# Kernel tuning notes

Hardware: AMD Instinct MI355X
Metric: run time of the kernel (lower is better)

## Reference

```python
import jax, jax.numpy as jnp
import numpy as np
from jax import lax

NMS_RADIUS = 3
DN = ('NCHW', 'OIHW', 'NCHW')


def _conv(x, w, b):
    # 3x3 or 1x1 conv, stride 1, SAME padding (matches padding=k//2 in torch)
    return lax.conv_general_dilated(x, w, (1, 1), 'SAME', dimension_numbers=DN) + b[None, :, None, None]


def _pool2(x):
    # 2x2 max pool, stride 2
    return lax.reduce_window(x, -jnp.inf, lax.max, (1, 1, 2, 2), (1, 1, 2, 2), 'VALID')


def simple_nms(scores, nms_radius):
    # scores: [b, H, W]. Iterative max-pool based NMS (2 suppression rounds).
    k = 2 * nms_radius + 1

    def mp(x):
        return lax.reduce_window(x, -jnp.inf, lax.max, (1, k, k), (1, 1, 1), 'SAME')

    zeros = jnp.zeros_like(scores)
    max_mask = scores == mp(scores)
    for _ in range(2):
        supp_mask = mp(max_mask.astype(scores.dtype)) > 0
        supp_scores = jnp.where(supp_mask, zeros, scores)
        new_max_mask = supp_scores == mp(supp_scores)
        max_mask = max_mask | (new_max_mask & ~supp_mask)
    return jnp.where(max_mask, scores, zeros)


def _forward(image, w1a, b1a, w1b, b1b, w2a, b2a, w2b, b2b, w3a, b3a, w3b, b3b,
             w4a, b4a, w4b, b4b, wPa, bPa, wPb, bPb, wDa, bDa, wDb, bDb):
    r = jax.nn.relu
    x = r(_conv(image, w1a, b1a)); x = r(_conv(x, w1b, b1b)); x = _pool2(x)
    x = r(_conv(x, w2a, b2a)); x = r(_conv(x, w2b, b2b)); x = _pool2(x)
    x = r(_conv(x, w3a, b3a)); x = r(_conv(x, w3b, b3b)); x = _pool2(x)
    x = r(_conv(x, w4a, b4a)); x = r(_conv(x, w4b, b4b))
    # detector head
    cPa = r(_conv(x, wPa, bPa))
    sc = _conv(cPa, wPb, bPb)                       # [b, 65, h, w]
    sc = jax.nn.softmax(sc, axis=1)[:, :-1]        # drop dustbin -> [b, 64, h, w]
    b, _, h, w = sc.shape
    sc = sc.transpose(0, 2, 3, 1).reshape(b, h, w, 8, 8)
    sc = sc.transpose(0, 1, 3, 2, 4).reshape(b, h * 8, w * 8)  # full-res score map
    # (bilinear interpolate to (ih, iw) with align_corners is identity since ih=h*8, iw=w*8)
    nms_scores = simple_nms(sc, NMS_RADIUS)
    # descriptor head
    cDa = r(_conv(x, wDa, bDa))
    desc = _conv(cDa, wDb, bDb)                    # [b, 256, h, w]
    desc = desc / jnp.linalg.norm(desc, axis=1, keepdims=True)
    return sc, nms_scores, desc


def setup_inputs():
    key = jax.random.key(0)
    ks = iter(jax.random.split(key, 32))
    image = jax.random.uniform(next(ks), (8, 1, 480, 640), dtype=jnp.float32)

    def cw(k, o, i, s):
        return jax.random.normal(k, (o, i, s, s), dtype=jnp.float32) * (0.5 / np.sqrt(i * s * s))

    c1, c2, c3, c4, c5 = 64, 64, 128, 128, 256
    inp = {'image': image}
    specs = [('1a', c1, 1, 3), ('1b', c1, c1, 3), ('2a', c2, c1, 3), ('2b', c2, c2, 3),
             ('3a', c3, c2, 3), ('3b', c3, c3, 3), ('4a', c4, c3, 3), ('4b', c4, c4, 3),
             ('Pa', c5, c4, 3), ('Pb', 65, c5, 1), ('Da', c5, c4, 3), ('Db', 256, c5, 1)]
    for name, o, i, s in specs:
        inp['w' + name] = cw(next(ks), o, i, s)
        inp['b' + name] = jax.random.normal(next(ks), (o,), dtype=jnp.float32) * 0.01
    return inp


def reference(image, w1a, b1a, w1b, b1b, w2a, b2a, w2b, b2b, w3a, b3a, w3b, b3b,
              w4a, b4a, w4b, b4b, wPa, bPa, wPb, bPb, wDa, bDa, wDb, bDb):
    return _forward(image, w1a, b1a, w1b, b1b, w2a, b2a, w2b, b2b, w3a, b3a, w3b, b3b,
                    w4a, b4a, w4b, b4b, wPa, bPa, wPb, bPb, wDa, bDa, wDb, bDb)
```

## Files before the change

### kernel.cpp

```cpp
#include <hip/hip_runtime.h>
#include <math.h>

typedef __attribute__((ext_vector_type(8))) _Float16 f16x8;
typedef __attribute__((ext_vector_type(4))) float f32x4;

__device__ __forceinline__ void f32_split(float x, ushort& h, ushort& l) {
    _Float16 hh = (_Float16)x;
    float r = x - (float)hh;
    _Float16 ll = (_Float16)r;
    union { _Float16 f; ushort u; } a, b;
    a.f = hh; b.f = ll;
    h = a.u; l = b.u;
}
__device__ __forceinline__ float h2f(ushort u) {
    union { ushort u; _Float16 f; } v; v.u = u; return (float)v.f;
}

__global__ void wtr_kernel(const float* __restrict__ src, ushort* __restrict__ dhi,
                           ushort* __restrict__ dlo, int CO, int CI)
{
    int n = CO * CI * 9, coci = CO * CI;
    for (int idx = blockIdx.x * 256 + threadIdx.x; idx < n; idx += gridDim.x * 256) {
        int tp = idx / coci, r = idx % coci;
        int co = r / CI, ci = r % CI;
        ushort h, l;
        f32_split(src[((size_t)co * CI + ci) * 9 + tp], h, l);
        dhi[idx] = h; dlo[idx] = l;
    }
}

template<int CI, int MW, int NW, int NR, bool POOL, bool FUSE1A>
__global__ __launch_bounds__(MW * NW * 64, 2) void mconv5_kernel(
    const ushort* __restrict__ in, size_t ipl,
    const float* __restrict__ image, const float* __restrict__ w1a,
    const float* __restrict__ b1a,
    const ushort* __restrict__ whi, const ushort* __restrict__ wlo,
    const float* __restrict__ bias,
    ushort* __restrict__ out, size_t opl,
    int H, int W, int COT, int TXC,
    int iy0, int inr, int y_start, int y_lim, int oy0, int onr)
{
    constexpr int BS = MW * NW * 64;
    constexpr int HALO = (MW * 8 + 2) * 10;
    __shared__ __align__(16) ushort AHI[HALO * 64];
    __shared__ __align__(16) ushort ALO[HALO * 64];
    __shared__ float fshared[FUSE1A ? 880 : 4];

    int t = threadIdx.x;
    int tx = blockIdx.x % TXC, ty = blockIdx.x / TXC;
    int x0 = tx * 8, y0 = y_start + ty * (MW * 8);
    int co0 = blockIdx.y * (NW * NR * 16);
    int b = blockIdx.z;

    int lane = t & 63, wid = t >> 6;
    int wm = wid / NW, wn = wid % NW;
    int fr = lane & 15, fg = lane >> 4;

    int hpx[4];
    #pragma unroll
    for (int mi = 0; mi < 4; ++mi) {
        int p = wm * 64 + mi * 16 + fr;
        hpx[mi] = (p >> 3) * 10 + (p & 7);
    }
    size_t wro[NR];
    #pragma unroll
    for (int nj = 0; nj < NR; ++nj) {
        int cog = co0 + wn * NR * 16 + nj * 16 + fr;
        wro[nj] = (size_t)cog * CI + fg * 8;
    }

    f32x4 acc[4][NR];
    #pragma unroll
    for (int nj = 0; nj < NR; ++nj) {
        float bv = bias[co0 + wn * NR * 16 + nj * 16 + fr];
        #pragma unroll
        for (int mi = 0; mi < 4; ++mi)
            acc[mi][nj] = f32x4{bv, bv, bv, bv};
    }

    const int NC = CI / 64;
    for (int cc = 0; cc < NC; ++cc) {
        if (cc > 0) __syncthreads();
        if constexpr (FUSE1A) {
            float* img_s = fshared;
            float* w1a_s = fshared + 240;
            float* b1a_s = fshared + 816;
            for (int idx = t; idx < 240; idx += BS) {
                int iy = idx / 12, ix = idx % 12;
                int gy = y0 - 2 + iy, gx = x0 - 2 + ix;
                img_s[idx] = (gy >= 0 && gy < H && gx >= 0 && gx < W)
                                 ? image[((size_t)b * H + gy) * W + gx] : 0.f;
            }
            for (int idx = t; idx < 576; idx += BS) w1a_s[idx] = w1a[idx];
            if (t < 64) b1a_s[t] = b1a[t];
            __syncthreads();
            for (int idx = t; idx < HALO * 8; idx += BS) {
                int hp = idx >> 3, g = idx & 7;
                int hpy = hp / 10, hpx2 = hp - hpy * 10;
                int gy = y0 - 1 + hpy, gx = x0 - 1 + hpx2;
                union { ushort u[8]; int4 v; } hu, lu;
                if (gy >= 0 && gy < H && gx >= 0 && gx < W) {
                    float iv[9];
                    #pragma unroll
                    for (int ky = 0; ky < 3; ++ky)
                        #pragma unroll
                        for (int kx = 0; kx < 3; ++kx)
                            iv[ky * 3 + kx] = img_s[(hpy + ky) * 12 + hpx2 + kx];
                    #pragma unroll
                    for (int j = 0; j < 8; ++j) {
                        int c = g * 8 + j;
                        float s = b1a_s[c];
                        const float* wc = &w1a_s[c * 9];
                        #pragma unroll
                        for (int k = 0; k < 9; ++k) s = fmaf(iv[k], wc[k], s);
                        f32_split(fmaxf(s, 0.f), hu.u[j], lu.u[j]);
                    }
                } else {
                    hu.v = make_int4(0, 0, 0, 0);
                    lu.v = make_int4(0, 0, 0, 0);
                }
                int base = hp * 64 + ((g ^ (hp & 7)) << 3);
                *reinterpret_cast<int4*>(&AHI[base]) = hu.v;
                *reinterpret_cast<int4*>(&ALO[base]) = lu.v;
            }
        } else {
            for (int idx = t; idx < HALO * 8; idx += BS) {
                int hp = idx >> 3, c8 = idx & 7;
                int hy = y0 - 1 + hp / 10, hx = x0 - 1 + hp % 10;
                int4 vh = make_int4(0, 0, 0, 0), vl = make_int4(0, 0, 0, 0);
                if (hy >= iy0 && hy < iy0 + inr && hx >= 0 && hx < W) {
                    size_t a = (((size_t)b * inr + (hy - iy0)) * W + hx) * CI + cc * 64 + c8 * 8;
                    vh = *reinterpret_cast<const int4*>(&in[a]);
                    vl = *reinterpret_cast<const int4*>(&in[a + ipl]);
                }
                int base = hp * 64 + ((c8 ^ (hp & 7)) << 3);
                *reinterpret_cast<int4*>(&AHI[base]) = vh;
                *reinterpret_cast<int4*>(&ALO[base]) = vl;
            }
        }

        size_t ccoff = (size_t)cc * 64;
        f16x8 whA[NR], wlA[NR], whB[NR], wlB[NR];
        {
            const ushort* wtH = whi + ccoff;
            const ushort* wtL = wlo + ccoff;
            #pragma unroll
            for (int nj = 0; nj < NR; ++nj) {
                whA[nj] = *reinterpret_cast<const f16x8*>(&wtH[wro[nj]]);
                wlA[nj] = *reinterpret_cast<const f16x8*>(&wtL[wro[nj]]);
            }
        }
        __syncthreads();

        #pragma unroll 1
        for (int tap = 0; tap < 9; ++tap) {
            {
                const ushort* wtH = whi + (size_t)tap * COT * CI + ccoff + 32;
                const ushort* wtL = wlo + (size_t)tap * COT * CI + ccoff + 32;
                #pragma unroll
                for (int nj = 0; nj < NR; ++nj) {
                    whB[nj] = *reinterpret_cast<const f16x8*>(&wtH[wro[nj]]);
                    wlB[nj] = *reinterpret_cast<const f16x8*>(&wtL[wro[nj]]);
                }
            }
            int ky = tap / 3, kx = tap - ky * 3;
            {
                f16x8 ah[4], al[4];
                #pragma unroll
                for (int mi = 0; mi < 4; ++mi) {
                    int hp = hpx[mi] + ky * 10 + kx;
                    int slot = fg ^ (hp & 7);
                    ah[mi] = *reinterpret_cast<const f16x8*>(&AHI[hp * 64 + slot * 8]);
                    al[mi] = *reinterpret_cast<const f16x8*>(&ALO[hp * 64 + slot * 8]);
                }
                #pragma unroll
                for (int mi = 0; mi < 4; ++mi)
                    #pragma unroll
                    for (int nj = 0; nj < NR; ++nj) {
                        acc[mi][nj] = __builtin_amdgcn_mfma_f32_16x16x32_f16(
                            ah[mi], whA[nj], acc[mi][nj], 0, 0, 0);
                        acc[mi][nj] = __builtin_amdgcn_mfma_f32_16x16x32_f16(
                            al[mi], whA[nj], acc[mi][nj], 0, 0, 0);
                        acc[mi][nj] = __builtin_amdgcn_mfma_f32_16x16x32_f16(
                            ah[mi], wlA[nj], acc[mi][nj], 0, 0, 0);
                    }
            }
            if (tap < 8) {
                const ushort* wtH = whi + (size_t)(tap + 1) * COT * CI + ccoff;
                const ushort* wtL = wlo + (size_t)(tap + 1) * COT * CI + ccoff;
                #pragma unroll
                for (int nj = 0; nj < NR; ++nj) {
                    whA[nj] = *reinterpret_cast<const f16x8*>(&wtH[wro[nj]]);
                    wlA[nj] = *reinterpret_cast<const f16x8*>(&wtL[wro[nj]]);
                }
            }
            {
                f16x8 ah[4], al[4];
                #pragma unroll
                for (int mi = 0; mi < 4; ++mi) {
                    int hp = hpx[mi] + ky * 10 + kx;
                    int slot = (4 + fg) ^ (hp & 7);
                    ah[mi] = *reinterpret_cast<const f16x8*>(&AHI[hp * 64 + slot * 8]);
                    al[mi] = *reinterpret_cast<const f16x8*>(&ALO[hp * 64 + slot * 8]);
                }
                #pragma unroll
                for (int mi = 0; mi < 4; ++mi)
                    #pragma unroll
                    for (int nj = 0; nj < NR; ++nj) {
                        acc[mi][nj] = __builtin_amdgcn_mfma_f32_16x16x32_f16(
                            ah[mi], whB[nj], acc[mi][nj], 0, 0, 0);
                        acc[mi][nj] = __builtin_amdgcn_mfma_f32_16x16x32_f16(
                            al[mi], whB[nj], acc[mi][nj], 0, 0, 0);
                        acc[mi][nj] = __builtin_amdgcn_mfma_f32_16x16x32_f16(
                            ah[mi], wlB[nj], acc[mi][nj], 0, 0, 0);
                    }
            }
        }
    }

    if constexpr (POOL) {
        int Wp = W >> 1;
        #pragma unroll
        for (int mi = 0; mi < 4; ++mi) {
            int qy = (y0 >> 1) + wm * 4 + mi;
            #pragma unroll
            for (int nj = 0; nj < NR; ++nj) {
                f32x4 v = acc[mi][nj];
                float v0 = fmaxf(v[0], 0.f), v1 = fmaxf(v[1], 0.f);
                float v2 = fmaxf(v[2], 0.f), v3 = fmaxf(v[3], 0.f);
                float mA = fmaxf(v0, v1), mB = fmaxf(v2, v3);
                float pA = fmaxf(mA, __shfl_xor(mA, 32));
                float pB = fmaxf(mB, __shfl_xor(mB, 32));
                if ((fg & 2) == 0 && qy < y_lim) {
                    int qx = (x0 >> 1) + (fg & 1) * 2;
                    int cog = co0 + wn * NR * 16 + nj * 16 + fr;
                    size_t oa = (((size_t)b * onr + (qy - oy0)) * Wp + qx) * COT + cog;
                    ushort h, l;
                    f32_split(pA, h, l);
                    out[oa] = h; out[oa + opl] = l;
                    f32_split(pB, h, l);
                    out[oa + COT] = h; out[oa + COT + opl] = l;
                }
            }
        }
    } else {
        #pragma unroll
        for (int mi = 0; mi < 4; ++mi)
            #pragma unroll
            for (int r = 0; r < 4; ++r) {
                int gy = y0 + wm * 8 + mi * 2 + (fg >> 1);
                int gx = x0 + (fg & 1) * 4 + r;
                if (gy < y_lim) {
                    size_t base = (((size_t)b * onr + (gy - oy0)) * W + gx) * COT;
                    #pragma unroll
                    for (int nj = 0; nj < NR; ++nj) {
                        int cog = co0 + wn * NR * 16 + nj * 16 + fr;
                        ushort h, l;
                        f32_split(fmaxf(acc[mi][nj][r], 0.f), h, l);
                        out[base + cog] = h;
                        out[base + cog + opl] = l;
                    }
                }
            }
    }
}

__global__ __launch_bounds__(256) void scores_kernel(
    const ushort* __restrict__ cpa, size_t cpl, const float* __restrict__ wpb,
    const float* __restrict__ bpb, float* __restrict__ sc)
{
    __shared__ __align__(16) float wT[128][66];
    __shared__ __align__(16) float xs[4][256];
    int t = threadIdx.x;
    int wave = t >> 6, lane = t & 63;
    int p = blockIdx.x * 4 + wave;

    ushort4 xh = *reinterpret_cast<const ushort4*>(&cpa[(size_t)p * 256 + lane * 4]);
    ushort4 xl = *reinterpret_cast<const ushort4*>(&cpa[(size_t)p * 256 + lane * 4 + cpl]);
    xs[wave][lane * 4 + 0] = h2f(xh.x) + h2f(xl.x);
    xs[wave][lane * 4 + 1] = h2f(xh.y) + h2f(xl.y);
    xs[wave][lane * 4 + 2] = h2f(xh.z) + h2f(xl.z);
    xs[wave][lane * 4 + 3] = h2f(xh.w) + h2f(xl.w);

    float a = bpb[lane];
    float a2 = bpb[64];
    for (int k0 = 0; k0 < 256; k0 += 128) {
        __syncthreads();
        for (int idx = t; idx < 65 * 128; idx += 256) {
            int o = idx / 128, i = idx % 128;
            wT[i][o] = wpb[o * 256 + k0 + i];
        }
        __syncthreads();
        for (int i = 0; i < 128; ++i) {
            float xb = xs[wave][k0 + i];
            a  = fmaf(xb, wT[i][lane], a);
            a2 = fmaf(xb, wT[i][64], a2);
        }
    }
    float m = a;
    #pragma unroll
    for (int off = 32; off; off >>= 1) m = fmaxf(m, __shfl_xor(m, off));
    m = fmaxf(m, a2);
    float e = expf(a - m);
    float s = e;
    #pragma unroll
    for (int off = 32; off; off >>= 1) s += __shfl_xor(s, off);
    s += expf(a2 - m);
    float r = e / s;
    int b = p / 4800, hw = p % 4800, h = hw / 80, w = hw % 80;
    int rr = lane >> 3, cc = lane & 7;
    sc[b * 307200 + (h * 8 + rr) * 640 + (w * 8 + cc)] = r;
}

#define NMS_STAGE(SRC)                                                        \
    __shared__ float ts[22][23];                                              \
    const int H = 480, W = 640;                                               \
    int bx = blockIdx.x * 16, by = blockIdx.y * 16, b = blockIdx.z;           \
    int t = threadIdx.x;                                                      \
    for (int idx = t; idx < 22 * 22; idx += 256) {                            \
        int yy = idx / 22, xx = idx % 22;                                     \
        int gy = by + yy - 3, gx = bx + xx - 3;                               \
        ts[yy][xx] = (gy >= 0 && gy < H && gx >= 0 && gx < W)                 \
                         ? (SRC)[b * 307200 + gy * W + gx] : -INFINITY;       \
    }                                                                         \
    __syncthreads();                                                          \
    int lx = t & 15, ly = t >> 4;                                             \
    float mx = -INFINITY;                                                     \
    _Pragma("unroll")                                                         \
    for (int dy = 0; dy < 7; ++dy)                                            \
        _Pragma("unroll")                                                     \
        for (int dx = 0; dx < 7; ++dx)                                       \
            mx = fmaxf(mx, ts[ly + dy][lx + dx]);                            \
    int p = b * 307200 + (by + ly) * W + (bx + lx);

__global__ __launch_bounds__(256) void nms_max_mask(
    const float* __restrict__ s, float* __restrict__ M)
{
    NMS_STAGE(s)
    M[p] = (ts[ly + 3][lx + 3] == mx) ? 1.f : 0.f;
}

__global__ __launch_bounds__(256) void nms_supp(
    const float* __restrict__ M, const float* __restrict__ s,
    float* __restrict__ supp, float* __restrict__ ss)
{
    NMS_STAGE(M)
    float sup = (mx > 0.f) ? 1.f : 0.f;
    supp[p] = sup;
    ss[p] = (sup > 0.f) ? 0.f : s[p];
}

template<bool LAST>
__global__ __launch_bounds__(256) void nms_update(
    const float* __restrict__ ssb, const float* __restrict__ supp,
    const float* __restrict__ s, float* __restrict__ M, float* __restrict__ outp)
{
    NMS_STAGE(ssb)
    bool new_max = (ts[ly + 3][lx + 3] == mx);
    float mo = M[p];
    float sp = supp[p];
    bool mn = (mo > 0.f) || (new_max && sp == 0.f);
    if (LAST)
        outp[p] = mn ? s[p] : 0.f;
    else
        M[p] = mn ? 1.f : 0.f;
}

__global__ __launch_bounds__(256, 2) void descdb_kernel(
    const ushort* __restrict__ cda, size_t cpl, const float* __restrict__ wdb,
    const float* __restrict__ bdb, float* __restrict__ outp)
{
    __shared__ __align__(16) float Xs[16][65];
    __shared__ __align__(16) float Ws[16][257];
    int t = threadIdx.x;
    int m0 = blockIdx.x * 64;
    int n_id = t & 31, m_id = t >> 5;

    float acc[8][8];
    #pragma unroll
    for (int nn = 0; nn < 8; ++nn) {
        float bv = bdb[n_id + 32 * nn];
        #pragma unroll
        for (int mm = 0; mm < 8; ++mm) acc[mm][nn] = bv;
    }

    for (int k0 = 0; k0 < 256; k0 += 16) {
        __syncthreads();
        for (int idx = t; idx < 64 * 16; idx += 256) {
            int m = idx / 16, k = idx % 16;
            size_t a = (size_t)(m0 + m) * 256 + k0 + k;
            Xs[k][m] = h2f(cda[a]) + h2f(cda[a + cpl]);
        }
        for (int idx = t; idx < 256 * 16; idx += 256) {
            int o = idx / 16, k = idx % 16;
            Ws[k][o] = wdb[o * 256 + k0 + k];
        }
        __syncthreads();
        #pragma unroll
        for (int k = 0; k < 16; ++k) {
            float xv[8], wv[8];
            #pragma unroll
            for (int mm = 0; mm < 8; ++mm) xv[mm] = Xs[k][m_id * 8 + mm];
            #pragma unroll
            for (int nn = 0; nn < 8; ++nn) wv[nn] = Ws[k][n_id + 32 * nn];
            #pragma unroll
            for (int mm = 0; mm < 8; ++mm)
                #pragma unroll
                for (int nn = 0; nn < 8; ++nn)
                    acc[mm][nn] = fmaf(xv[mm], wv[nn], acc[mm][nn]);
        }
    }
    #pragma unroll
    for (int mm = 0; mm < 8; ++mm) {
        float sq = 0.f;
        #pragma unroll
        for (int nn = 0; nn < 8; ++nn) sq = fmaf(acc[mm][nn], acc[mm][nn], sq);
        #pragma unroll
        for (int off = 16; off; off >>= 1) sq += __shfl_xor(sq, off);
        float inv = 1.f / sqrtf(sq);
        int P = m0 + m_id * 8 + mm;
        int b = P / 4800, hw = P % 4800;
        #pragma unroll
        for (int nn = 0; nn < 8; ++nn) {
            int o = n_id + 32 * nn;
            outp[(b * 256 + o) * 4800 + hw] = acc[mm][nn] * inv;
        }
    }
}

extern "C" void kernel_launch(void* const* d_in, const int* in_sizes, int n_in,
                              void* d_out, int out_size, void* d_ws, size_t ws_size,
                              hipStream_t stream)
{
    const float* image = (const float*)d_in[0];
    const float* w1a = (const float*)d_in[1];  const float* b1a = (const float*)d_in[2];
    const float* w1b = (const float*)d_in[3];  const float* b1b = (const float*)d_in[4];
    const float* w2a = (const float*)d_in[5];  const float* b2a = (const float*)d_in[6];
    const float* w2b = (const float*)d_in[7];  const float* b2b = (const float*)d_in[8];
    const float* w3a = (const float*)d_in[9];  const float* b3a = (const float*)d_in[10];
    const float* w3b = (const float*)d_in[11]; const float* b3b = (const float*)d_in[12];
    const float* w4a = (const float*)d_in[13]; const float* b4a = (const float*)d_in[14];
    const float* w4b = (const float*)d_in[15]; const float* b4b = (const float*)d_in[16];
    const float* wPa = (const float*)d_in[17]; const float* bPa = (const float*)d_in[18];
    const float* wPb = (const float*)d_in[19]; const float* bPb = (const float*)d_in[20];
    const float* wDa = (const float*)d_in[21]; const float* bDa = (const float*)d_in[22];
    const float* wDb = (const float*)d_in[23]; const float* bDb = (const float*)d_in[24];

    float* out_sc   = (float*)d_out;
    float* out_nms  = out_sc + 2457600;
    float* out_desc = out_sc + 4915200;

    ushort* U = (ushort*)d_ws;
    const int O1B = 0, O2A = 36864, O2B = 73728, O3A = 110592, O3B = 184320,
              O4A = 331776, O4B = 479232, OPA = 626688, ODA = 921600;
    const size_t TOT = 1216512;
    ushort* Whi = U;
    ushort* Wlo = U + TOT;
    ushort* A1  = U + 2500000;
    ushort* A2  = U + 42000000;
    ushort* A3  = U + 2500000;
    ushort* A4  = U + 42000000;
    ushort* A5  = U + 2500000;
    ushort* A6  = U + 13000000;
    ushort* A7  = U + 23000000;
    ushort* cPa = U + 33000000;
    ushort* cDa = U + 33000000;
    float* nmsMb  = (float*)(U + 54000000);
    float* nmsSup = nmsMb + 2457600;
    float* nmsSs  = nmsSup + 2457600;

    struct WE { const float* w; int off, co, ci; };
    WE WL[9] = {{w1b, O1B, 64, 64},  {w2a, O2A, 64, 64},  {w2b, O2B, 64, 64},
                {w3a, O3A, 128, 64}, {w3b, O3B, 128, 128},{w4a, O4A, 128, 128},
                {w4b, O4B, 128, 128},{wPa, OPA, 256, 128},{wDa, ODA, 256, 128}};
    for (int i = 0; i < 9; ++i) {
        int n = WL[i].co * WL[i].ci * 9;
        wtr_kernel<<<(n + 255) / 256, 256, 0, stream>>>(
            WL[i].w, Whi + WL[i].off, Wlo + WL[i].off, WL[i].co, WL[i].ci);
    }

    const size_t P1 = 39321600, P2 = 39321600, P3 = 9830400,
                 P4 = 19660800, P5 = 4915200, PP = 9830400;

    mconv5_kernel<64, 2, 2, 2, true, true><<<dim3(80 * 30, 1, 8), 256, 0, stream>>>(
        nullptr, 0, image, w1a, b1a, Whi + O1B, Wlo + O1B, b1b,
        A1, P1, 480, 640, 64, 80, 0, 480, 0, 240, 0, 240);
    mconv5_kernel<64, 2, 1, 4, false, false><<<dim3(40 * 15, 1, 8), 128, 0, stream>>>(
        A1, P1, nullptr, nullptr, nullptr, Whi + O2A, Wlo + O2A, b2a,
        A2, P2, 240, 320, 64, 40, 0, 240, 0, 240, 0, 240);
    mconv5_kernel<64, 2, 1, 4, true, false><<<dim3(40 * 15, 1, 8), 128, 0, stream>>>(
        A2, P2, nullptr, nullptr, nullptr, Whi + O2B, Wlo + O2B, b2b,
        A3, P3, 240, 320, 64, 40, 0, 240, 0, 120, 0, 120);

    mconv5_kernel<64, 2, 2, 4, false, false><<<dim3(20 * 8, 1, 8), 256, 0, stream>>>(
        A3, P3, nullptr, nullptr, nullptr, Whi + O3A, Wlo + O3A, b3a,
        A4, P4, 120, 160, 128, 20, 0, 120, 0, 120, 0, 120);
    mconv5_kernel<128, 2, 2, 4, true, false><<<dim3(20 * 8, 1, 8), 256, 0, stream>>>(
        A4, P4, nullptr, nullptr, nullptr, Whi + O3B, Wlo + O3B, b3b,
        A5, P5, 120, 160, 128, 20, 0, 120, 0, 60, 0, 60);

    mconv5_kernel<128, 2, 2, 4, false, false><<<dim3(10 * 4, 1, 8), 256, 0, stream>>>(
        A5, P5, nullptr, nullptr, nullptr, Whi + O4A, Wlo + O4A, b4a,
        A6, P5, 60, 80, 128, 10, 0, 60, 0, 60, 0, 60);
    mconv5_kernel<128, 2, 2, 4, false, false><<<dim3(10 * 4, 1, 8), 256, 0, stream>>>(
        A6, P5, nullptr, nullptr, nullptr, Whi + O4B, Wlo + O4B, b4b,
        A7, P5, 60, 80, 128, 10, 0, 60, 0, 60, 0, 60);

    mconv5_kernel<128, 2, 2, 4, false, false><<<dim3(10 * 4, 2, 8), 256, 0, stream>>>(
        A7, P5, nullptr, nullptr, nullptr, Whi + OPA, Wlo + OPA, bPa,
        cPa, PP, 60, 80, 256, 10, 0, 60, 0, 60, 0, 60);
    scores_kernel<<<9600, 256, 0, stream>>>(cPa, PP, wPb, bPb, out_sc);

    nms_max_mask<<<dim3(40, 30, 8), 256, 0, stream>>>(out_sc, nmsMb);
    nms_supp<<<dim3(40, 30, 8), 256, 0, stream>>>(nmsMb, out_sc, nmsSup, nmsSs);
    nms_update<false><<<dim3(40, 30, 8), 256, 0, stream>>>(nmsSs, nmsSup, out_sc, nmsMb, out_nms);
    nms_supp<<<dim3(40, 30, 8), 256, 0, stream>>>(nmsMb, out_sc, nmsSup, nmsSs);
    nms_update<true><<<dim3(40, 30, 8), 256, 0, stream>>>(nmsSs, nmsSup, out_sc, nmsMb, out_nms);

    mconv5_kernel<128, 2, 2, 4, false, false><<<dim3(10 * 4, 2, 8), 256, 0, stream>>>(
        A7, P5, nullptr, nullptr, nullptr, Whi + ODA, Wlo + ODA, bDa,
        cDa, PP, 60, 80, 256, 10, 0, 60, 0, 60, 0, 60);
    descdb_kernel<<<600, 256, 0, stream>>>(cDa, PP, wDb, bDb, out_desc);
}
```

Before: 2.170 ms.

## Halve conv LDS footprint by staging lo activation half in registers for a second pass

The split-fp16 conv kernel used to keep both the hi and lo activation halves in shared memory. Now it keeps only one buffer: it first runs the hi-activation MFMAs (hi*whi and hi*wlo), then writes the lo half, held in registers meanwhile, into the same buffer and runs a second tap loop for lo*whi. This halves LDS per block, and the launch-bounds minimum occupancy is raised to 4 for 256-thread configs. In exchange it adds an extra barrier pair, re-reads the weights in the second pass, and adds register pressure from the staged values.

```diff
diff --git a/kernel.cpp b/kernel.cpp
--- a/kernel.cpp
+++ b/kernel.cpp
@@ -30,7 +30,7 @@
 }
 
 template<int CI, int MW, int NW, int NR, bool POOL, bool FUSE1A>
-__global__ __launch_bounds__(MW * NW * 64, 2) void mconv5_kernel(
+__global__ __launch_bounds__(MW * NW * 64, (MW * NW == 4) ? 4 : 2) void mconv6_kernel(
     const ushort* __restrict__ in, size_t ipl,
     const float* __restrict__ image, const float* __restrict__ w1a,
     const float* __restrict__ b1a,
@@ -42,8 +42,8 @@
 {
     constexpr int BS = MW * NW * 64;
     constexpr int HALO = (MW * 8 + 2) * 10;
-    __shared__ __align__(16) ushort AHI[HALO * 64];
-    __shared__ __align__(16) ushort ALO[HALO * 64];
+    constexpr int NST = (HALO * 8 + BS - 1) / BS;
+    __shared__ __align__(16) ushort A[HALO * 64];
     __shared__ float fshared[FUSE1A ? 880 : 4];
 
     int t = threadIdx.x;
@@ -81,6 +81,7 @@
     const int NC = CI / 64;
     for (int cc = 0; cc < NC; ++cc) {
         if (cc > 0) __syncthreads();
+        int4 rlo[NST];
         if constexpr (FUSE1A) {
             float* img_s = fshared;
             float* w1a_s = fshared + 240;
@@ -94,48 +95,56 @@
             for (int idx = t; idx < 576; idx += BS) w1a_s[idx] = w1a[idx];
             if (t < 64) b1a_s[t] = b1a[t];
             __syncthreads();
-            for (int idx = t; idx < HALO * 8; idx += BS) {
-                int hp = idx >> 3, g = idx & 7;
-                int hpy = hp / 10, hpx2 = hp - hpy * 10;
-                int gy = y0 - 1 + hpy, gx = x0 - 1 + hpx2;
-                union { ushort u[8]; int4 v; } hu, lu;
-                if (gy >= 0 && gy < H && gx >= 0 && gx < W) {
-                    float iv[9];
-                    #pragma unroll
-                    for (int ky = 0; ky < 3; ++ky)
+            #pragma unroll
+            for (int s = 0; s < NST; ++s) {
+                int idx = t + s * BS;
+                if (idx < HALO * 8) {
+                    int hp = idx >> 3, g = idx & 7;
+                    int hpy = hp / 10, hpx2 = hp - hpy * 10;
+                    int gy = y0 - 1 + hpy, gx = x0 - 1 + hpx2;
+                    union { ushort u[8]; int4 v; } hu, lu;
+                    if (gy >= 0 && gy < H && gx >= 0 && gx < W) {
+                        float iv[9];
                         #pragma unroll
-                        for (int kx = 0; kx < 3; ++kx)
-                            iv[ky * 3 + kx] = img_s[(hpy + ky) * 12 + hpx2 + kx];
-                    #pragma unroll
-                    for (int j = 0; j < 8; ++j) {
-                        int c = g * 8 + j;
-                        float s = b1a_s[c];
-                        const float* wc = &w1a_s[c * 9];
+                        for (int ky = 0; ky < 3; ++ky)
+                            #pragma unroll
+                            for (int kx = 0; kx < 3; ++kx)
+                                iv[ky * 3 + kx] = img_s[(hpy + ky) * 12 + hpx2 + kx];
                         #pragma unroll
-                        for (int k = 0; k < 9; ++k) s = fmaf(iv[k], wc[k], s);
-                        f32_split(fmaxf(s, 0.f), hu.u[j], lu.u[j]);
+                        for (int j = 0; j < 8; ++j) {
+                            int c = g * 8 + j;
+                            float s2 = b1a_s[c];
+                            const float* wc = &w1a_s[c * 9];
+                            #pragma unroll
+                            for (int k = 0; k < 9; ++k) s2 = fmaf(iv[k], wc[k], s2);
+                            f32_split(fmaxf(s2, 0.f), hu.u[j], lu.u[j]);
+                        }
+                    } else {
+                        hu.v = make_int4(0, 0, 0, 0);
+                        lu.v = make_int4(0, 0, 0, 0);
                     }
-                } else {
-                    hu.v = make_int4(0, 0, 0, 0);
-                    lu.v = make_int4(0, 0, 0, 0);
-                }
-                int base = hp * 64 + ((g ^ (hp & 7)) << 3);
-                *reinterpret_cast<int4*>(&AHI[base]) = hu.v;
-                *reinterpret_cast<int4*>(&ALO[base]) = lu.v;
+                    int base = hp * 64 + ((g ^ (hp & 7)) << 3);
+                    *reinterpret_cast<int4*>(&A[base]) = hu.v;
+                    rlo[s] = lu.v;
+                }
             }
         } else {
-            for (int idx = t; idx < HALO * 8; idx += BS) {
-                int hp = idx >> 3, c8 = idx & 7;
-                int hy = y0 - 1 + hp / 10, hx = x0 - 1 + hp % 10;
-                int4 vh = make_int4(0, 0, 0, 0), vl = make_int4(0, 0, 0, 0);
-                if (hy >= iy0 && hy < iy0 + inr && hx >= 0 && hx < W) {
-                    size_t a = (((size_t)b * inr + (hy - iy0)) * W + hx) * CI + cc * 64 + c8 * 8;
-                    vh = *reinterpret_cast<const int4*>(&in[a]);
-                    vl = *reinterpret_cast<const int4*>(&in[a + ipl]);
-                }
-                int base = hp * 64 + ((c8 ^ (hp & 7)) << 3);
-                *reinterpret_cast<int4*>(&AHI[base]) = vh;
-                *reinterpret_cast<int4*>(&ALO[base]) = vl;
+            #pragma unroll
+            for (int s = 0; s < NST; ++s) {
+                int idx = t + s * BS;
+                if (idx < HALO * 8) {
+                    int hp = idx >> 3, c8 = idx & 7;
+                    int hy = y0 - 1 + hp / 10, hx = x0 - 1 + hp % 10;
+                    int4 vh = make_int4(0, 0, 0, 0), vl = make_int4(0, 0, 0, 0);
+                    if (hy >= iy0 && hy < iy0 + inr && hx >= 0 && hx < W) {
+                        size_t a = (((size_t)b * inr + (hy - iy0)) * W + hx) * CI + cc * 64 + c8 * 8;
+                        vh = *reinterpret_cast<const int4*>(&in[a]);
+                        vl = *reinterpret_cast<const int4*>(&in[a + ipl]);
+                    }
+                    int base = hp * 64 + ((c8 ^ (hp & 7)) << 3);
+                    *reinterpret_cast<int4*>(&A[base]) = vh;
+                    rlo[s] = vl;
+                }
             }
         }
 
@@ -165,13 +174,12 @@
             }
             int ky = tap / 3, kx = tap - ky * 3;
             {
-                f16x8 ah[4], al[4];
+                f16x8 ah[4];
                 #pragma unroll
                 for (int mi = 0; mi < 4; ++mi) {
                     int hp = hpx[mi] + ky * 10 + kx;
                     int slot = fg ^ (hp & 7);
-                    ah[mi] = *reinterpret_cast<const f16x8*>(&AHI[hp * 64 + slot * 8]);
-                    al[mi] = *reinterpret_cast<const f16x8*>(&ALO[hp * 64 + slot * 8]);
+                    ah[mi] = *reinterpret_cast<const f16x8*>(&A[hp * 64 + slot * 8]);
                 }
                 #pragma unroll
                 for (int mi = 0; mi < 4; ++mi)
@@ -180,8 +188,6 @@
                         acc[mi][nj] = __builtin_amdgcn_mfma_f32_16x16x32_f16(
                             ah[mi], whA[nj], acc[mi][nj], 0, 0, 0);
                         acc[mi][nj] = __builtin_amdgcn_mfma_f32_16x16x32_f16(
-                            al[mi], whA[nj], acc[mi][nj], 0, 0, 0);
-                        acc[mi][nj] = __builtin_amdgcn_mfma_f32_16x16x32_f16(
                             ah[mi], wlA[nj], acc[mi][nj], 0, 0, 0);
                     }
             }
@@ -195,13 +201,12 @@
                 }
             }
             {
-                f16x8 ah[4], al[4];
+                f16x8 ah[4];
                 #pragma unroll
                 for (int mi = 0; mi < 4; ++mi) {
                     int hp = hpx[mi] + ky * 10 + kx;
                     int slot = (4 + fg) ^ (hp & 7);
-                    ah[mi] = *reinterpret_cast<const f16x8*>(&AHI[hp * 64 + slot * 8]);
-                    al[mi] = *reinterpret_cast<const f16x8*>(&ALO[hp * 64 + slot * 8]);
+                    ah[mi] = *reinterpret_cast<const f16x8*>(&A[hp * 64 + slot * 8]);
                 }
                 #pragma unroll
                 for (int mi = 0; mi < 4; ++mi)
@@ -210,10 +215,73 @@
                         acc[mi][nj] = __builtin_amdgcn_mfma_f32_16x16x32_f16(
                             ah[mi], whB[nj], acc[mi][nj], 0, 0, 0);
                         acc[mi][nj] = __builtin_amdgcn_mfma_f32_16x16x32_f16(
-                            al[mi], whB[nj], acc[mi][nj], 0, 0, 0);
-                        acc[mi][nj] = __builtin_amdgcn_mfma_f32_16x16x32_f16(
                             ah[mi], wlB[nj], acc[mi][nj], 0, 0, 0);
                     }
+            }
+        }
+
+        __syncthreads();
+        #pragma unroll
+        for (int s = 0; s < NST; ++s) {
+            int idx = t + s * BS;
+            if (idx < HALO * 8) {
+                int hp = idx >> 3, c8 = idx & 7;
+                int base = hp * 64 + ((c8 ^ (hp & 7)) << 3);
+                *reinterpret_cast<int4*>(&A[base]) = rlo[s];
+            }
+        }
+        {
+            const ushort* wtH = whi + ccoff;
+            #pragma unroll
+            for (int nj = 0; nj < NR; ++nj)
+                whA[nj] = *reinterpret_cast<const f16x8*>(&wtH[wro[nj]]);
+        }
+        __syncthreads();
+
+        #pragma unroll 1
+        for (int tap = 0; tap < 9; ++tap) {
+            {
+                const ushort* wtH = whi + (size_t)tap * COT * CI + ccoff + 32;
+                #pragma unroll
+                for (int nj = 0; nj < NR; ++nj)
+                    whB[nj] = *reinterpret_cast<const f16x8*>(&wtH[wro[nj]]);
+            }
+            int ky = tap / 3, kx = tap - ky * 3;
+            {
+                f16x8 al[4];
+                #pragma unroll
+                for (int mi = 0; mi < 4; ++mi) {
+                    int hp = hpx[mi] + ky * 10 + kx;
+                    int slot = fg ^ (hp & 7);
+                    al[mi] = *reinterpret_cast<const f16x8*>(&A[hp * 64 + slot * 8]);
+                }
+                #pragma unroll
+                for (int mi = 0; mi < 4; ++mi)
+                    #pragma unroll
+                    for (int nj = 0; nj < NR; ++nj)
+                        acc[mi][nj] = __builtin_amdgcn_mfma_f32_16x16x32_f16(
+                            al[mi], whA[nj], acc[mi][nj], 0, 0, 0);
+            }
+            if (tap < 8) {
+                const ushort* wtH = whi + (size_t)(tap + 1) * COT * CI + ccoff;
+                #pragma unroll
+                for (int nj = 0; nj < NR; ++nj)
+                    whA[nj] = *reinterpret_cast<const f16x8*>(&wtH[wro[nj]]);
+            }
+            {
+                f16x8 al[4];
+                #pragma unroll
+                for (int mi = 0; mi < 4; ++mi) {
+                    int hp = hpx[mi] + ky * 10 + kx;
+                    int slot = (4 + fg) ^ (hp & 7);
+                    al[mi] = *reinterpret_cast<const f16x8*>(&A[hp * 64 + slot * 8]);
+                }
+                #pragma unroll
+                for (int mi = 0; mi < 4; ++mi)
+                    #pragma unroll
+                    for (int nj = 0; nj < NR; ++nj)
+                        acc[mi][nj] = __builtin_amdgcn_mfma_f32_16x16x32_f16(
+                            al[mi], whB[nj], acc[mi][nj], 0, 0, 0);
             }
         }
     }
@@ -482,31 +550,31 @@
     const size_t P1 = 39321600, P2 = 39321600, P3 = 9830400,
                  P4 = 19660800, P5 = 4915200, PP = 9830400;
 
-    mconv5_kernel<64, 2, 2, 2, true, true><<<dim3(80 * 30, 1, 8), 256, 0, stream>>>(
+    mconv6_kernel<64, 2, 2, 2, true, true><<<dim3(80 * 30, 1, 8), 256, 0, stream>>>(
         nullptr, 0, image, w1a, b1a, Whi + O1B, Wlo + O1B, b1b,
         A1, P1, 480, 640, 64, 80, 0, 480, 0, 240, 0, 240);
-    mconv5_kernel<64, 2, 1, 4, false, false><<<dim3(40 * 15, 1, 8), 128, 0, stream>>>(
+    mconv6_kernel<64, 2, 1, 4, false, false><<<dim3(40 * 15, 1, 8), 128, 0, stream>>>(
         A1, P1, nullptr, nullptr, nullptr, Whi + O2A, Wlo + O2A, b2a,
         A2, P2, 240, 320, 64, 40, 0, 240, 0, 240, 0, 240);
-    mconv5_kernel<64, 2, 1, 4, true, false><<<dim3(40 * 15, 1, 8), 128, 0, stream>>>(
+    mconv6_kernel<64, 2, 1, 4, true, false><<<dim3(40 * 15, 1, 8), 128, 0, stream>>>(
         A2, P2, nullptr, nullptr, nullptr, Whi + O2B, Wlo + O2B, b2b,
         A3, P3, 240, 320, 64, 40, 0, 240, 0, 120, 0, 120);
 
-    mconv5_kernel<64, 2, 2, 4, false, false><<<dim3(20 * 8, 1, 8), 256, 0, stream>>>(
+    mconv6_kernel<64, 2, 2, 4, false, false><<<dim3(20 * 8, 1, 8), 256, 0, stream>>>(
         A3, P3, nullptr, nullptr, nullptr, Whi + O3A, Wlo + O3A, b3a,
         A4, P4, 120, 160, 128, 20, 0, 120, 0, 120, 0, 120);
-    mconv5_kernel<128, 2, 2, 4, true, false><<<dim3(20 * 8, 1, 8), 256, 0, stream>>>(
+    mconv6_kernel<128, 2, 2, 4, true, false><<<dim3(20 * 8, 1, 8), 256, 0, stream>>>(
         A4, P4, nullptr, nullptr, nullptr, Whi + O3B, Wlo + O3B, b3b,
         A5, P5, 120, 160, 128, 20, 0, 120, 0, 60, 0, 60);
 
-    mconv5_kernel<128, 2, 2, 4, false, false><<<dim3(10 * 4, 1, 8), 256, 0, stream>>>(
+    mconv6_kernel<128, 2, 2, 4, false, false><<<dim3(10 * 4, 1, 8), 256, 0, stream>>>(
         A5, P5, nullptr, nullptr, nullptr, Whi + O4A, Wlo + O4A, b4a,
         A6, P5, 60, 80, 128, 10, 0, 60, 0, 60, 0, 60);
-    mconv5_kernel<128, 2, 2, 4, false, false><<<dim3(10 * 4, 1, 8), 256, 0, stream>>>(
+    mconv6_kernel<128, 2, 2, 4, false, false><<<dim3(10 * 4, 1, 8), 256, 0, stream>>>(
         A6, P5, nullptr, nullptr, nullptr, Whi + O4B, Wlo + O4B, b4b,
         A7, P5, 60, 80, 128, 10, 0, 60, 0, 60, 0, 60);
 
-    mconv5_kernel<128, 2, 2, 4, false, false><<<dim3(10 * 4, 2, 8), 256, 0, stream>>>(
+    mconv6_kernel<128, 2, 2, 4, false, false><<<dim3(10 * 4, 2, 8), 256, 0, stream>>>(
         A7, P5, nullptr, nullptr, nullptr, Whi + OPA, Wlo + OPA, bPa,
         cPa, PP, 60, 80, 256, 10, 0, 60, 0, 60, 0, 60);
     scores_kernel<<<9600, 256, 0, stream>>>(cPa, PP, wPb, bPb, out_sc);
@@ -517,7 +585,7 @@
     nms_supp<<<dim3(40, 30, 8), 256, 0, stream>>>(nmsMb, out_sc, nmsSup, nmsSs);
     nms_update<true><<<dim3(40, 30, 8), 256, 0, stream>>>(nmsSs, nmsSup, out_sc, nmsMb, out_nms);
 
-    mconv5_kernel<128, 2, 2, 4, false, false><<<dim3(10 * 4, 2, 8), 256, 0, stream>>>(
+    mconv6_kernel<128, 2, 2, 4, false, false><<<dim3(10 * 4, 2, 8), 256, 0, stream>>>(
         A7, P5, nullptr, nullptr, nullptr, Whi + ODA, Wlo + ODA, bDa,
         cDa, PP, 60, 80, 256, 10, 0, 60, 0, 60, 0, 60);
     descdb_kernel<<<600, 256, 0, stream>>>(cDa, PP, wDb, bDb, out_desc);
```

Measured after the change: 3.613 ms. 1.67x slower.
